# Performance work log

Hardware: AMD Instinct MI355X
Metric: run time of the kernel (lower is better)

Reference implementation:

```python
import jax, jax.numpy as jnp
import numpy as np

N_NODES = 50000
N_EDGES = 600000
D_IN = 128
D_OUT = 128


def setup_inputs() -> dict:
    key = jax.random.key(0)
    k1, k2, k3, k4 = jax.random.split(key, 4)
    x = jax.random.normal(k1, (N_NODES, D_IN), dtype=jnp.float32)
    edge_index = jax.random.randint(k2, (2, N_EDGES), 0, N_NODES, dtype=jnp.int64)
    edge_weight = jax.random.uniform(k3, (N_EDGES,), dtype=jnp.float32)
    W = jax.random.normal(k4, (D_IN, D_OUT), dtype=jnp.float32) * (1.0 / np.sqrt(D_IN))
    b = jnp.zeros((D_OUT,), dtype=jnp.float32)
    return {"x": x, "edge_index": edge_index, "edge_weight": edge_weight, "W": W, "b": b}


def reference(x, edge_index, edge_weight, W, b):
    # GCNConv (PyG semantics): add self-loops, symmetric deg^{-1/2} normalization,
    # linear transform, scatter-add to targets, bias; then ReLU. Dropout is
    # identity in eval mode.
    n = x.shape[0]
    loop = jnp.arange(n, dtype=edge_index.dtype)
    src = jnp.concatenate([edge_index[0], loop])  # message sources
    dst = jnp.concatenate([edge_index[1], loop])  # aggregation targets
    ew = jnp.concatenate([edge_weight, jnp.ones((n,), dtype=x.dtype)])
    # weighted in-degree on targets
    deg = jax.ops.segment_sum(ew, dst, num_segments=n)
    dinv = jnp.where(deg > 0, jax.lax.rsqrt(deg), jnp.zeros_like(deg))
    norm = dinv[src] * ew * dinv[dst]  # [E+N]
    h = x @ W  # [N, D_OUT]
    msg = h[src] * norm[:, None]  # [E+N, D_OUT]
    out = jax.ops.segment_sum(msg, dst, num_segments=n) + b
    return jax.nn.relu(out)
```

## Files before the change

kernel.cpp:

```cpp
#include <hip/hip_runtime.h>

#define N_NODES 50000
#define N_EDGES 600000
#define D 128
#define SCAN_B 256
#define NB ((N_NODES + SCAN_B - 1) / SCAN_B)
#define REP 4
#define FXSHIFT 44
#define GEMM_BLOCKS ((N_NODES + 63) / 64)
#define FILL_BLOCKS ((N_EDGES + 255) / 256)
#define GATHER_GROUPS ((N_NODES + 3) / 4)
#define ZERO_BLOCKS 392

typedef __attribute__((ext_vector_type(8))) short short8;
typedef __attribute__((ext_vector_type(4))) float f32x4;
typedef unsigned long long u64;

__device__ __forceinline__ ushort f2bf(float f) {
    unsigned u = __float_as_uint(f);
    unsigned r = (u + 0x7FFFu + ((u >> 16) & 1u)) >> 16;
    return (ushort)r;
}
__device__ __forceinline__ float bf2f(ushort h) {
    return __uint_as_float(((unsigned)h) << 16);
}

__device__ __forceinline__ void wfrag_body(int t, const float* __restrict__ W,
                                           ushort* __restrict__ wfh,
                                           ushort* __restrict__ wfl) {
    int lane = t & 63;
    int ks   = (t >> 6) & 3;
    int ct   = t >> 8;
    int n  = ct * 16 + (lane & 15);
    int k0 = ks * 32 + (lane >> 4) * 8;
    ushort hv[8], lv[8];
#pragma unroll
    for (int j = 0; j < 8; ++j) {
        float v = W[(k0 + j) * D + n];
        ushort hh = f2bf(v);
        hv[j] = hh;
        lv[j] = f2bf(v - bf2f(hh));
    }
    size_t base = (((size_t)ct * 4 + ks) * 64 + lane) * 8;
#pragma unroll
    for (int j = 0; j < 8; ++j) { wfh[base + j] = hv[j]; wfl[base + j] = lv[j]; }
}

__global__ void prep_kernel(ulonglong2* __restrict__ zp, int n2,
                            const float* __restrict__ W,
                            ushort* __restrict__ wfh, ushort* __restrict__ wfl) {
    if (blockIdx.x < ZERO_BLOCKS) {
        int i = blockIdx.x * 256 + threadIdx.x;
        if (i < n2) zp[i] = make_ulonglong2(0ull, 0ull);
    } else {
        wfrag_body((blockIdx.x - ZERO_BLOCKS) * 256 + threadIdx.x, W, wfh, wfl);
    }
}

__global__ void deg_cnt_kernel(const int* __restrict__ dst,
                               const float* __restrict__ ew,
                               u64* __restrict__ degp) {
    int e = blockIdx.x * 256 + threadIdx.x;
    if (e < N_EDGES) {
        int d = dst[e];
        int r = blockIdx.x & (REP - 1);
        u64 fx = (u64)llrintf(ew[e] * 16777216.0f);
        atomicAdd(&degp[(size_t)d * REP + r], (1ull << FXSHIFT) | fx);
    }
}

__global__ void scan_fused_kernel(const u64* __restrict__ degp,
                                  float* __restrict__ dinv,
                                  int* __restrict__ off,
                                  int* __restrict__ cursor,
                                  u64* __restrict__ flags) {
    __shared__ int s[SCAN_B];
    __shared__ int sbase_sh;
    int t = threadIdx.x;
    int i = blockIdx.x * SCAN_B + t;
    int v = 0;
    u64 pr[REP];
    if (i < N_NODES) {
        u64 fxsum = 0;
        int c = 0;
        const u64* dp = degp + (size_t)i * REP;
#pragma unroll
        for (int r = 0; r < REP; ++r) {
            pr[r] = dp[r];
            fxsum += pr[r] & ((1ull << FXSHIFT) - 1);
            c += (int)(pr[r] >> FXSHIFT);
        }
        dinv[i] = rsqrtf(1.0f + (float)fxsum * (1.0f / 16777216.0f));
        v = c;
    }
    s[t] = v;
    __syncthreads();
    for (int o = 1; o < SCAN_B; o <<= 1) {
        int x = (t >= o) ? s[t - o] : 0;
        __syncthreads();
        s[t] += x;
        __syncthreads();
    }
    int localExcl = s[t] - v;
    int blockSum  = s[SCAN_B - 1];

    if (t == 0) {
        __hip_atomic_store(&flags[blockIdx.x], (1ull << 62) | (u64)blockSum,
                           __ATOMIC_RELEASE, __HIP_MEMORY_SCOPE_AGENT);
    }
    if (t < 64) {
        u64 sum = 0;
        for (int j0 = 0; j0 < (int)blockIdx.x; j0 += 64) {
            int j = j0 + t;
            u64 f = 0;
            if (j < (int)blockIdx.x) {
                do {
                    f = __hip_atomic_load(&flags[j], __ATOMIC_ACQUIRE,
                                          __HIP_MEMORY_SCOPE_AGENT);
                } while (f == 0ull);
            }
            sum += f & ((1ull << 62) - 1);
        }
#pragma unroll
        for (int o = 32; o > 0; o >>= 1)
            sum += (u64)__shfl_xor((long long)sum, o);
        if (t == 0) sbase_sh = (int)sum;
    }
    __syncthreads();

    if (i < N_NODES) {
        int o = localExcl + sbase_sh;
        off[i] = o;
        int run = o;
        int* cp = cursor + (size_t)i * REP;
#pragma unroll
        for (int r = 0; r < REP; ++r) {
            cp[r] = run;
            run += (int)(pr[r] >> FXSHIFT);
        }
    }
    if (i == 0) off[N_NODES] = N_EDGES;
}

__global__ __launch_bounds__(256) void gemm_kernel(
        const float* __restrict__ x,
        const ushort* __restrict__ wfh, const ushort* __restrict__ wfl,
        ushort* __restrict__ hbf) {
    __shared__ __attribute__((aligned(16))) ushort xh[64 * 128];
    __shared__ __attribute__((aligned(16))) ushort wsh[16384];
    __shared__ __attribute__((aligned(16))) ushort wsl[16384];

    int t  = threadIdx.x;
    int r0 = blockIdx.x * 64;

#pragma unroll
    for (int p = 0; p < 8; ++p) {
        int idx = p * 256 + t;
        ((short8*)wsh)[idx] = ((const short8*)wfh)[idx];
        ((short8*)wsl)[idx] = ((const short8*)wfl)[idx];
    }
#pragma unroll
    for (int p = 0; p < 8; ++p) {
        int row  = p * 8 + (t >> 5);
        int g    = t & 31;
        int grow = r0 + row;
        float4 v = make_float4(0.f, 0.f, 0.f, 0.f);
        if (grow < N_NODES) v = ((const float4*)(x + (size_t)grow * D))[g];
        ushort4 hi;
        hi.x = f2bf(v.x); hi.y = f2bf(v.y); hi.z = f2bf(v.z); hi.w = f2bf(v.w);
        int bo = (row * 256 + g * 8) ^ ((row & 7) << 4);
        *(ushort4*)((char*)xh + bo) = hi;
    }
    __syncthreads();

    int w  = t >> 6;
    int l  = t & 63;
    int m  = l & 15;
    int gq = l >> 4;

    f32x4 acc[8];
#pragma unroll
    for (int ct = 0; ct < 8; ++ct) acc[ct] = (f32x4){0.f, 0.f, 0.f, 0.f};

#pragma unroll
    for (int ks = 0; ks < 4; ++ks) {
        int row = w * 16 + m;
        int bo  = (row * 256 + gq * 16 + ks * 64) ^ ((row & 7) << 4);
        short8 ah = *(const short8*)((const char*)xh + bo);
#pragma unroll
        for (int ct = 0; ct < 8; ++ct) {
            int fb = ((ct * 4 + ks) * 64 + l);
            short8 bh = ((const short8*)wsh)[fb];
            short8 bl = ((const short8*)wsl)[fb];
            acc[ct] = __builtin_amdgcn_mfma_f32_16x16x32_bf16(ah, bh, acc[ct], 0, 0, 0);
            acc[ct] = __builtin_amdgcn_mfma_f32_16x16x32_bf16(ah, bl, acc[ct], 0, 0, 0);
        }
    }

    int orow0 = r0 + w * 16 + gq * 4;
#pragma unroll
    for (int ct = 0; ct < 8; ++ct) {
#pragma unroll
        for (int r = 0; r < 4; ++r) {
            int row = orow0 + r;
            if (row < N_NODES) hbf[(size_t)row * D + ct * 16 + m] = f2bf(acc[ct][r]);
        }
    }
}

__global__ void fill_kernel(const int* __restrict__ src, const int* __restrict__ dst,
                            const float* __restrict__ ew, const float* __restrict__ dinv,
                            int* __restrict__ cursor, u64* __restrict__ edge_s) {
    int e = blockIdx.x * 256 + threadIdx.x;
    if (e >= N_EDGES) return;
    int s = src[e];
    int d = dst[e];
    int r = blockIdx.x & (REP - 1);
    int pos = atomicAdd(&cursor[(size_t)d * REP + r], 1);
    float w = ew[e] * dinv[s] * dinv[d];
    edge_s[pos] = ((u64)__float_as_uint(w) << 32) | (unsigned)s;
}

__global__ __launch_bounds__(256) void gather_kernel(
        const int* __restrict__ off, const u64* __restrict__ edge_s,
        const float* __restrict__ dinv,
        const ushort* __restrict__ hbf, const float* __restrict__ bias,
        float* __restrict__ out) {
    int node = blockIdx.x * 4 + (threadIdx.x >> 6);
    if (node >= N_NODES) return;
    int lane = threadIdx.x & 63;
    int q  = lane >> 4;
    int fl = lane & 15;

    int begin = off[node];
    int end   = off[node + 1];
    float dd  = dinv[node];
    float sw  = dd * dd;

    float acc[8] = {0.f, 0.f, 0.f, 0.f, 0.f, 0.f, 0.f, 0.f};

    short8 sv = ((const short8*)(hbf + (size_t)node * D))[fl];
    if (q == 0) {
#pragma unroll
        for (int j = 0; j < 8; ++j) acc[j] = bf2f((ushort)sv[j]) * sw;
    }

    for (int j0 = begin; j0 < end; j0 += 64) {
        int nc = end - j0;
        if (nc > 64) nc = 64;
        u64 p = 0;
        if (lane < nc) p = edge_s[j0 + lane];
        int iters = (nc + 3) >> 2;
#pragma unroll 2
        for (int k = 0; k < iters; ++k) {
            int ei = k * 4 + q;
            u64 pe = __shfl((long long)p, ei);
            bool valid = ei < nc;
            int   ss = valid ? (int)(pe & 0xFFFFFFFFu) : 0;
            float ww = valid ? __uint_as_float((unsigned)(pe >> 32)) : 0.0f;
            short8 v = ((const short8*)(hbf + (size_t)ss * D))[fl];
#pragma unroll
            for (int j = 0; j < 8; ++j)
                acc[j] = fmaf(bf2f((ushort)v[j]), ww, acc[j]);
        }
    }

#pragma unroll
    for (int j = 0; j < 8; ++j) {
        acc[j] += __shfl_xor(acc[j], 16);
        acc[j] += __shfl_xor(acc[j], 32);
    }

    if (q == 0) {
        float4 b1 = ((const float4*)bias)[fl * 2];
        float4 b2 = ((const float4*)bias)[fl * 2 + 1];
        float4 o1 = make_float4(fmaxf(acc[0] + b1.x, 0.f), fmaxf(acc[1] + b1.y, 0.f),
                                fmaxf(acc[2] + b1.z, 0.f), fmaxf(acc[3] + b1.w, 0.f));
        float4 o2 = make_float4(fmaxf(acc[4] + b2.x, 0.f), fmaxf(acc[5] + b2.y, 0.f),
                                fmaxf(acc[6] + b2.z, 0.f), fmaxf(acc[7] + b2.w, 0.f));
        ((float4*)(out + (size_t)node * D))[fl * 2]     = o1;
        ((float4*)(out + (size_t)node * D))[fl * 2 + 1] = o2;
    }
}

extern "C" void kernel_launch(void* const* d_in, const int* in_sizes, int n_in,
                              void* d_out, int out_size, void* d_ws, size_t ws_size,
                              hipStream_t stream) {
    const float* x  = (const float*)d_in[0];
    const int*   ei = (const int*)d_in[1];
    const float* ew = (const float*)d_in[2];
    const float* W  = (const float*)d_in[3];
    const float* bias = (const float*)d_in[4];
    float*       out = (float*)d_out;

    const int* src = ei;
    const int* dst = ei + N_EDGES;

    ushort* hbf    = (ushort*)d_ws;
    u64*    degp   = (u64*)(hbf + (size_t)N_NODES * D);
    u64*    flags  = degp + (size_t)REP * N_NODES;
    float*  dinv   = (float*)(flags + 256);
    int*    off    = (int*)(dinv + N_NODES);
    int*    cursor = off + (N_NODES + 2);
    u64*    edge_s = (u64*)(cursor + (size_t)REP * N_NODES);
    ushort* wfh    = (ushort*)(edge_s + N_EDGES);
    ushort* wfl    = wfh + 16384;
    size_t need = ((size_t)(wfl + 16384) - (size_t)d_ws);
    if (ws_size < need) return;

    int n2 = (int)(((size_t)REP * N_NODES * 8 + 256 * 8) / 16);
    prep_kernel<<<ZERO_BLOCKS + 8, 256, 0, stream>>>((ulonglong2*)degp, n2,
                                                     W, wfh, wfl);
    deg_cnt_kernel<<<FILL_BLOCKS, 256, 0, stream>>>(dst, ew, degp);
    scan_fused_kernel<<<NB, SCAN_B, 0, stream>>>(degp, dinv, off, cursor, flags);
    gemm_kernel<<<GEMM_BLOCKS, 256, 0, stream>>>(x, wfh, wfl, hbf);
    fill_kernel<<<FILL_BLOCKS, 256, 0, stream>>>(src, dst, ew, dinv, cursor, edge_s);
    gather_kernel<<<GATHER_GROUPS, 256, 0, stream>>>(off, edge_s, dinv,
                                                     hbf, bias, out);
}
```

Baseline: 123.8 us.

## Fuse GEMM and edge fill into one launch, drop bf16 low-part split

Merges the GEMM and the CSR fill kernel into a single launch whose blocks branch by index, so the independent fill work can overlap the GEMM and one launch is saved. It also drops the hi/lo bf16 split of W, halving the MFMA count and removing the low-part fragment buffer. W fragments are now read straight from global memory instead of being staged in LDS. The cost is lower GEMM accuracy (single bf16 W), and the fused kernel's register and LDS footprint now also applies to the lightweight fill blocks.

```diff
diff --git a/kernel.cpp b/kernel.cpp
--- a/kernel.cpp
+++ b/kernel.cpp
@@ -26,34 +26,28 @@
 }
 
 __device__ __forceinline__ void wfrag_body(int t, const float* __restrict__ W,
-                                           ushort* __restrict__ wfh,
-                                           ushort* __restrict__ wfl) {
+                                           ushort* __restrict__ wfh) {
     int lane = t & 63;
     int ks   = (t >> 6) & 3;
     int ct   = t >> 8;
     int n  = ct * 16 + (lane & 15);
     int k0 = ks * 32 + (lane >> 4) * 8;
-    ushort hv[8], lv[8];
-#pragma unroll
-    for (int j = 0; j < 8; ++j) {
-        float v = W[(k0 + j) * D + n];
-        ushort hh = f2bf(v);
-        hv[j] = hh;
-        lv[j] = f2bf(v - bf2f(hh));
-    }
+    ushort hv[8];
+#pragma unroll
+    for (int j = 0; j < 8; ++j) hv[j] = f2bf(W[(k0 + j) * D + n]);
     size_t base = (((size_t)ct * 4 + ks) * 64 + lane) * 8;
 #pragma unroll
-    for (int j = 0; j < 8; ++j) { wfh[base + j] = hv[j]; wfl[base + j] = lv[j]; }
+    for (int j = 0; j < 8; ++j) wfh[base + j] = hv[j];
 }
 
 __global__ void prep_kernel(ulonglong2* __restrict__ zp, int n2,
                             const float* __restrict__ W,
-                            ushort* __restrict__ wfh, ushort* __restrict__ wfl) {
+                            ushort* __restrict__ wfh) {
     if (blockIdx.x < ZERO_BLOCKS) {
         int i = blockIdx.x * 256 + threadIdx.x;
         if (i < n2) zp[i] = make_ulonglong2(0ull, 0ull);
     } else {
-        wfrag_body((blockIdx.x - ZERO_BLOCKS) * 256 + threadIdx.x, W, wfh, wfl);
+        wfrag_body((blockIdx.x - ZERO_BLOCKS) * 256 + threadIdx.x, W, wfh);
     }
 }
 
@@ -142,83 +136,75 @@
     if (i == 0) off[N_NODES] = N_EDGES;
 }
 
-__global__ __launch_bounds__(256) void gemm_kernel(
+__global__ __launch_bounds__(256) void fused_fg_kernel(
         const float* __restrict__ x,
-        const ushort* __restrict__ wfh, const ushort* __restrict__ wfl,
-        ushort* __restrict__ hbf) {
+        const ushort* __restrict__ wfh,
+        ushort* __restrict__ hbf,
+        const int* __restrict__ src, const int* __restrict__ dst,
+        const float* __restrict__ ew, const float* __restrict__ dinv,
+        int* __restrict__ cursor, u64* __restrict__ edge_s) {
     __shared__ __attribute__((aligned(16))) ushort xh[64 * 128];
-    __shared__ __attribute__((aligned(16))) ushort wsh[16384];
-    __shared__ __attribute__((aligned(16))) ushort wsl[16384];
-
-    int t  = threadIdx.x;
-    int r0 = blockIdx.x * 64;
-
-#pragma unroll
-    for (int p = 0; p < 8; ++p) {
-        int idx = p * 256 + t;
-        ((short8*)wsh)[idx] = ((const short8*)wfh)[idx];
-        ((short8*)wsl)[idx] = ((const short8*)wfl)[idx];
-    }
-#pragma unroll
-    for (int p = 0; p < 8; ++p) {
-        int row  = p * 8 + (t >> 5);
-        int g    = t & 31;
-        int grow = r0 + row;
-        float4 v = make_float4(0.f, 0.f, 0.f, 0.f);
-        if (grow < N_NODES) v = ((const float4*)(x + (size_t)grow * D))[g];
-        ushort4 hi;
-        hi.x = f2bf(v.x); hi.y = f2bf(v.y); hi.z = f2bf(v.z); hi.w = f2bf(v.w);
-        int bo = (row * 256 + g * 8) ^ ((row & 7) << 4);
-        *(ushort4*)((char*)xh + bo) = hi;
-    }
-    __syncthreads();
-
-    int w  = t >> 6;
-    int l  = t & 63;
-    int m  = l & 15;
-    int gq = l >> 4;
-
-    f32x4 acc[8];
-#pragma unroll
-    for (int ct = 0; ct < 8; ++ct) acc[ct] = (f32x4){0.f, 0.f, 0.f, 0.f};
-
-#pragma unroll
-    for (int ks = 0; ks < 4; ++ks) {
-        int row = w * 16 + m;
-        int bo  = (row * 256 + gq * 16 + ks * 64) ^ ((row & 7) << 4);
-        short8 ah = *(const short8*)((const char*)xh + bo);
+
+    int t = threadIdx.x;
+    int b = blockIdx.x;
+    if (b < GEMM_BLOCKS) {
+        int r0 = b * 64;
+#pragma unroll
+        for (int p = 0; p < 8; ++p) {
+            int row  = p * 8 + (t >> 5);
+            int g    = t & 31;
+            int grow = r0 + row;
+            float4 v = make_float4(0.f, 0.f, 0.f, 0.f);
+            if (grow < N_NODES) v = ((const float4*)(x + (size_t)grow * D))[g];
+            ushort4 hi;
+            hi.x = f2bf(v.x); hi.y = f2bf(v.y); hi.z = f2bf(v.z); hi.w = f2bf(v.w);
+            int bo = (row * 256 + g * 8) ^ ((row & 7) << 4);
+            *(ushort4*)((char*)xh + bo) = hi;
+        }
+        __syncthreads();
+
+        int w  = t >> 6;
+        int l  = t & 63;
+        int m  = l & 15;
+        int gq = l >> 4;
+
+        f32x4 acc[8];
+#pragma unroll
+        for (int ct = 0; ct < 8; ++ct) acc[ct] = (f32x4){0.f, 0.f, 0.f, 0.f};
+
+#pragma unroll
+        for (int ks = 0; ks < 4; ++ks) {
+            int row = w * 16 + m;
+            int bo  = (row * 256 + gq * 16 + ks * 64) ^ ((row & 7) << 4);
+            short8 ah = *(const short8*)((const char*)xh + bo);
+#pragma unroll
+            for (int ct = 0; ct < 8; ++ct) {
+                size_t fb = (((size_t)ct * 4 + ks) * 64 + l) * 8;
+                short8 bh = *(const short8*)(wfh + fb);
+                acc[ct] = __builtin_amdgcn_mfma_f32_16x16x32_bf16(ah, bh, acc[ct], 0, 0, 0);
+            }
+        }
+
+        int orow0 = r0 + w * 16 + gq * 4;
 #pragma unroll
         for (int ct = 0; ct < 8; ++ct) {
-            int fb = ((ct * 4 + ks) * 64 + l);
-            short8 bh = ((const short8*)wsh)[fb];
-            short8 bl = ((const short8*)wsl)[fb];
-            acc[ct] = __builtin_amdgcn_mfma_f32_16x16x32_bf16(ah, bh, acc[ct], 0, 0, 0);
-            acc[ct] = __builtin_amdgcn_mfma_f32_16x16x32_bf16(ah, bl, acc[ct], 0, 0, 0);
-        }
-    }
-
-    int orow0 = r0 + w * 16 + gq * 4;
-#pragma unroll
-    for (int ct = 0; ct < 8; ++ct) {
-#pragma unroll
-        for (int r = 0; r < 4; ++r) {
-            int row = orow0 + r;
-            if (row < N_NODES) hbf[(size_t)row * D + ct * 16 + m] = f2bf(acc[ct][r]);
-        }
-    }
-}
-
-__global__ void fill_kernel(const int* __restrict__ src, const int* __restrict__ dst,
-                            const float* __restrict__ ew, const float* __restrict__ dinv,
-                            int* __restrict__ cursor, u64* __restrict__ edge_s) {
-    int e = blockIdx.x * 256 + threadIdx.x;
-    if (e >= N_EDGES) return;
-    int s = src[e];
-    int d = dst[e];
-    int r = blockIdx.x & (REP - 1);
-    int pos = atomicAdd(&cursor[(size_t)d * REP + r], 1);
-    float w = ew[e] * dinv[s] * dinv[d];
-    edge_s[pos] = ((u64)__float_as_uint(w) << 32) | (unsigned)s;
+#pragma unroll
+            for (int r = 0; r < 4; ++r) {
+                int row = orow0 + r;
+                if (row < N_NODES) hbf[(size_t)row * D + ct * 16 + m] = f2bf(acc[ct][r]);
+            }
+        }
+    } else {
+        int fb = b - GEMM_BLOCKS;
+        int e = fb * 256 + t;
+        if (e >= N_EDGES) return;
+        int s = src[e];
+        int d = dst[e];
+        int r = fb & (REP - 1);
+        int pos = atomicAdd(&cursor[(size_t)d * REP + r], 1);
+        float w = ew[e] * dinv[s] * dinv[d];
+        edge_s[pos] = ((u64)__float_as_uint(w) << 32) | (unsigned)s;
+    }
 }
 
 __global__ __launch_bounds__(256) void gather_kernel(
@@ -304,17 +290,15 @@
     int*    cursor = off + (N_NODES + 2);
     u64*    edge_s = (u64*)(cursor + (size_t)REP * N_NODES);
     ushort* wfh    = (ushort*)(edge_s + N_EDGES);
-    ushort* wfl    = wfh + 16384;
-    size_t need = ((size_t)(wfl + 16384) - (size_t)d_ws);
+    size_t need = ((size_t)(wfh + 16384) - (size_t)d_ws);
     if (ws_size < need) return;
 
     int n2 = (int)(((size_t)REP * N_NODES * 8 + 256 * 8) / 16);
-    prep_kernel<<<ZERO_BLOCKS + 8, 256, 0, stream>>>((ulonglong2*)degp, n2,
-                                                     W, wfh, wfl);
+    prep_kernel<<<ZERO_BLOCKS + 8, 256, 0, stream>>>((ulonglong2*)degp, n2, W, wfh);
     deg_cnt_kernel<<<FILL_BLOCKS, 256, 0, stream>>>(dst, ew, degp);
     scan_fused_kernel<<<NB, SCAN_B, 0, stream>>>(degp, dinv, off, cursor, flags);
-    gemm_kernel<<<GEMM_BLOCKS, 256, 0, stream>>>(x, wfh, wfl, hbf);
-    fill_kernel<<<FILL_BLOCKS, 256, 0, stream>>>(src, dst, ew, dinv, cursor, edge_s);
+    fused_fg_kernel<<<GEMM_BLOCKS + FILL_BLOCKS, 256, 0, stream>>>(
+        x, wfh, hbf, src, dst, ew, dinv, cursor, edge_s);
     gather_kernel<<<GATHER_GROUPS, 256, 0, stream>>>(off, edge_s, dinv,
                                                      hbf, bias, out);
 }
```

New measurement: 108.8 us. -12.1%, faster.
